# Kernel tuning notes

Hardware: AMD Instinct MI355X
Metric: run time of the kernel (lower is better)

The kernel has to match this reference:

```python
import jax, jax.numpy as jnp
import numpy as np

N_NODES = 15000
N_EDGES = 60000
NODE_VOCAB = 118 + 20000
EDGE_VOCAB = 4 + 50
NODE_INDIM = 64
EDGE_INDIM = 32
H = 32          # node_hidden_feats
EH = 64         # edge_hidden_feats
NUM_STEPS = 3   # num_step_message_passing
N_BOND_TYPES = 4  # edge ids < 4 are chemical bonds -> edge_func1, else knowledge relations -> edge_func2


def setup_inputs() -> dict:
    key = jax.random.key(0)
    ks = jax.random.split(key, 20)
    s = 0.05  # param scale for numerical stability
    return {
        "node_ids": jax.random.randint(ks[0], (N_NODES,), 0, NODE_VOCAB),
        "edge_ids": jax.random.randint(ks[1], (N_EDGES,), 0, EDGE_VOCAB),
        "src": jax.random.randint(ks[2], (N_EDGES,), 0, N_NODES),
        "dst": jax.random.randint(ks[3], (N_EDGES,), 0, N_NODES),
        "node_table": jax.random.normal(ks[4], (NODE_VOCAB, NODE_INDIM), jnp.float32),
        "edge_table": jax.random.normal(ks[5], (EDGE_VOCAB, EDGE_INDIM), jnp.float32),
        "proj_W": jax.random.normal(ks[6], (H, NODE_INDIM), jnp.float32) * s,
        "proj_b": jnp.zeros((H,), jnp.float32),
        "attn_w": jax.random.normal(ks[7], (2 * H,), jnp.float32) * s,
        "e1_W1": jax.random.normal(ks[8], (EH, EDGE_INDIM), jnp.float32) * s,
        "e1_b1": jnp.zeros((EH,), jnp.float32),
        "e1_W2": jax.random.normal(ks[9], (H * H, EH), jnp.float32) * s,
        "e1_b2": jnp.zeros((H * H,), jnp.float32),
        "e2_W1": jax.random.normal(ks[10], (EH, EDGE_INDIM), jnp.float32) * s,
        "e2_b1": jnp.zeros((EH,), jnp.float32),
        "e2_W2": jax.random.normal(ks[11], (H * H, EH), jnp.float32) * s,
        "e2_b2": jnp.zeros((H * H,), jnp.float32),
        "gru_Wih": jax.random.normal(ks[12], (3 * H, H), jnp.float32) * s,
        "gru_Whh": jax.random.normal(ks[13], (3 * H, H), jnp.float32) * s,
        "gru_bih": jnp.zeros((3 * H,), jnp.float32),
        "gru_bhh": jnp.zeros((3 * H,), jnp.float32),
    }


def _edge_softmax(logits, dst, num_nodes):
    # softmax over incoming edges of each destination node
    m = jax.ops.segment_max(logits, dst, num_segments=num_nodes)
    ex = jnp.exp(logits - m[dst])
    s = jax.ops.segment_sum(ex, dst, num_segments=num_nodes)
    return ex / s[dst]


def reference(node_ids, edge_ids, src, dst, node_table, edge_table, proj_W, proj_b,
              attn_w, e1_W1, e1_b1, e1_W2, e1_b2, e2_W1, e2_b1, e2_W2, e2_b2,
              gru_Wih, gru_Whh, gru_bih, gru_bhh):
    # --- embedding lookups ---
    nf = node_table[node_ids]                      # [N, node_indim]
    ef = edge_table[edge_ids]                      # [E, edge_indim]
    # --- project node feats: Linear + ReLU ---
    h = jax.nn.relu(nf @ proj_W.T + proj_b)        # [N, H]

    # --- per-edge weight matrices from the two edge MLPs (edge feats are
    # constant across message-passing steps, so compute once) ---
    def edge_mlp(W1, b1, W2, b2):
        z = jax.nn.relu(ef @ W1.T + b1)            # [E, EH]
        return (z @ W2.T + b2).reshape(-1, H, H)   # [E, H, H]

    W_e1 = edge_mlp(e1_W1, e1_b1, e1_W2, e1_b2)
    W_e2 = edge_mlp(e2_W1, e2_b1, e2_W2, e2_b2)
    is_bond = (edge_ids < N_BOND_TYPES)[:, None, None]
    W_edge = jnp.where(is_bond, W_e1, W_e2)        # [E, H, H]

    hidden = h                                     # GRU hidden state (seq of len 1 -> GRUCell)
    for _ in range(NUM_STEPS):
        # attention logits on edges: leaky_relu(attn_fc([h_src || h_dst]))
        a = jax.nn.leaky_relu(
            h[src] @ attn_w[:H] + h[dst] @ attn_w[H:])     # [E]
        alpha = _edge_softmax(a, dst, N_NODES)             # [E]
        # edge-conditioned message: (h_src @ W_e) weighted by attention
        msg = jnp.einsum('ei,eio->eo', h[src], W_edge) * alpha[:, None]  # [E, H]
        agg = jax.ops.segment_sum(msg, dst, num_segments=N_NODES)       # [N, H]
        m = jax.nn.relu(agg)
        # single GRU step (torch nn.GRU, 1 layer, seq_len 1)
        gi = m @ gru_Wih.T + gru_bih               # [N, 3H]
        gh = hidden @ gru_Whh.T + gru_bhh          # [N, 3H]
        ir, iz, inn = jnp.split(gi, 3, axis=1)
        hr, hz, hn = jnp.split(gh, 3, axis=1)
        r = jax.nn.sigmoid(ir + hr)
        z = jax.nn.sigmoid(iz + hz)
        n = jnp.tanh(inn + r * hn)
        hidden = (1.0 - z) * n + z * hidden
        h = hidden
    return h
```

## Files before the change

kernel.cpp:

```cpp
#include <hip/hip_runtime.h>
#include <math.h>

#define N_NODES   15000
#define N_EDGES   60000
#define EVOCAB    54
#define NODE_INDIM 64
#define EDGE_INDIM 32
#define H  32
#define EH 64
#define N_BOND 4

#define NPB   8
#define NBLK  (N_NODES / NPB)
#define CAP   128

#define TASK_VOCAB (EVOCAB * 1024)
#define TASK_PROJ  (N_NODES * H)
#define TASK_EDGE_BASE (TASK_VOCAB + TASK_PROJ)
#define TA_TOTAL   (TASK_EDGE_BASE + N_EDGES)

#define WT_OFF   0
#define H0_OFF   221184
#define H1_OFF   2141184
#define W4_OFF   4061184
#define W2_OFF   4077568
#define LS0_OFF  4085760
#define BS0_OFF  4145760
#define LS1_OFF  4205760
#define BS1_OFF  4265760
#define CNT_OFF  4325760
#define EPK_OFF  4333440
#define W2T1_OFF 5293440
#define W2T2_OFF 5555584
#define PT_OFF   5817728

__global__ __launch_bounds__(256)
void pre_kernel(const float* __restrict__ e1_W2, const float* __restrict__ e2_W2,
                const float* __restrict__ proj_W,
                const float* __restrict__ gWih, const float* __restrict__ gWhh,
                float* __restrict__ W2T1, float* __restrict__ W2T2,
                float* __restrict__ PT,
                float4* __restrict__ Wpk4, float2* __restrict__ Wpk2,
                int* __restrict__ cnt)
{
    int b = blockIdx.x, tid = threadIdx.x;
    if (b < 32) {
        __shared__ float st[64][65];
        const float* in = (b < 16) ? e1_W2 : e2_W2;
        float* out      = (b < 16) ? W2T1  : W2T2;
        int f0 = (b & 15) * 64;
        #pragma unroll
        for (int it = 0; it < 16; ++it) {
            int idx = it * 256 + tid;
            int r = idx >> 6, c = idx & 63;
            st[r][c] = in[(f0 + r) * 64 + c];
        }
        __syncthreads();
        #pragma unroll
        for (int it = 0; it < 16; ++it) {
            int idx = it * 256 + tid;
            int k = idx >> 6, f = idx & 63;
            out[k * 1024 + f0 + f] = st[f][k];
        }
    } else if (b == 32) {
        __shared__ float sp2[64][33];
        #pragma unroll
        for (int it = 0; it < 8; ++it) {
            int idx = it * 256 + tid;
            int o = idx >> 6, j = idx & 63;
            sp2[j][o] = proj_W[idx];
        }
        __syncthreads();
        #pragma unroll
        for (int it = 0; it < 8; ++it) {
            int idx = it * 256 + tid;
            int j = idx >> 5, o = idx & 31;
            PT[idx] = sp2[j][o];
        }
    } else if (b <= 36) {
        int q = (b - 33) * 256 + tid;
        int j = q >> 5, o = q & 31;
        Wpk4[q] = make_float4(gWih[o * 32 + j], gWih[(32 + o) * 32 + j],
                              gWih[(64 + o) * 32 + j], gWhh[o * 32 + j]);
        Wpk2[q] = make_float2(gWhh[(32 + o) * 32 + j], gWhh[(64 + o) * 32 + j]);
    } else {
        #pragma unroll
        for (int it = 0; it < 8; ++it) {
            int idx = it * 256 + tid;
            if (idx < NBLK) cnt[idx] = 0;
        }
    }
}

__global__ __launch_bounds__(256)
void setup_kernel(const int* __restrict__ node_ids, const int* __restrict__ src,
                  const int* __restrict__ dst, const int* __restrict__ eid,
                  const float* __restrict__ node_table, const float* __restrict__ edge_table,
                  const float* __restrict__ PT, const float* __restrict__ proj_b,
                  const float* __restrict__ attn_w,
                  const float* __restrict__ e1_W1, const float* __restrict__ e1_b1,
                  const float* __restrict__ e1_b2,
                  const float* __restrict__ e2_W1, const float* __restrict__ e2_b1,
                  const float* __restrict__ e2_b2,
                  const float* __restrict__ W2T1, const float* __restrict__ W2T2,
                  float* __restrict__ Wt, float* __restrict__ h0,
                  float* __restrict__ ls, float* __restrict__ bs,
                  int* __restrict__ cnt, int* __restrict__ blkE)
{
    int t = blockIdx.x * 256 + threadIdx.x;
    if (t >= TA_TOTAL) return;
    if (t < TASK_VOCAB) {
        int v = t >> 10, f = t & 1023, l = t & 63;
        const float* W1  = (v < N_BOND) ? e1_W1 : e2_W1;
        const float* b1  = (v < N_BOND) ? e1_b1 : e2_b1;
        const float* b2  = (v < N_BOND) ? e1_b2 : e2_b2;
        const float* W2T = (v < N_BOND) ? W2T1  : W2T2;
        const float4* ef4 = (const float4*)(edge_table + v * EDGE_INDIM);
        const float4* w14 = (const float4*)(W1 + l * EDGE_INDIM);
        float z = b1[l];
        #pragma unroll
        for (int j = 0; j < 8; ++j) {
            float4 a = ef4[j], b = w14[j];
            z += a.x*b.x + a.y*b.y + a.z*b.z + a.w*b.w;
        }
        z = fmaxf(z, 0.f);
        float y = b2[f];
        #pragma unroll 16
        for (int k = 0; k < 64; ++k)
            y += __shfl(z, k, 64) * W2T[k * 1024 + f];
        Wt[(v << 10) + f] = y;
    } else if (t < TASK_EDGE_BASE) {
        int q = t - TASK_VOCAB;
        int n = q >> 5, o = q & 31;
        int gid = node_ids[n];
        const float* nf = node_table + (size_t)gid * NODE_INDIM;
        float nfa = nf[o], nfb = nf[32 + o];
        float acc = proj_b[o];
        #pragma unroll 8
        for (int j = 0; j < 32; ++j)
            acc += __shfl(nfa, j, 32) * PT[j * 32 + o];
        #pragma unroll 8
        for (int j = 0; j < 32; ++j)
            acc += __shfl(nfb, j, 32) * PT[(32 + j) * 32 + o];
        float hval = fmaxf(acc, 0.f);
        h0[q] = hval;
        float c1 = hval * attn_w[o], c2 = hval * attn_w[32 + o];
        #pragma unroll
        for (int k = 16; k > 0; k >>= 1) {
            c1 += __shfl_xor(c1, k, 32);
            c2 += __shfl_xor(c2, k, 32);
        }
        if (o == 0) { ls[n] = c1; bs[n] = c2; }
    } else {
        int e = t - TASK_EDGE_BASE;
        int d = dst[e];
        int blk = d >> 3;
        int pack = src[e] | (eid[e] << 14) | ((d & 7) << 20);
        int slot = atomicAdd(&cnt[blk], 1);
        if (slot < CAP) blkE[blk * CAP + slot] = pack;
    }
}

__global__ __launch_bounds__(256)
void mp_kernel(const int* __restrict__ cnt, const int* __restrict__ blkE,
               const float* __restrict__ hc, const float* __restrict__ Wt,
               const float* __restrict__ attn_w,
               const float4* __restrict__ Wpk4, const float2* __restrict__ Wpk2,
               const float* __restrict__ gbih, const float* __restrict__ gbhh,
               const float* __restrict__ lsc, const float* __restrict__ bsc,
               float* __restrict__ lsn, float* __restrict__ bsn,
               float* __restrict__ op, int last)
{
    __shared__ float4 smsg4[CAP * 8];
    __shared__ float  sexs[CAP];
    __shared__ int    spk[CAP];
    __shared__ float  sbs[NPB];

    int b = blockIdx.x, tid = threadIdx.x;
    int cntB = cnt[b];
    if (cntB > CAP) cntB = CAP;
    if (tid < cntB) spk[tid] = blkE[b * CAP + tid];
    if (tid < NPB)  sbs[tid] = bsc[(b << 3) + tid];
    __syncthreads();

    int g = tid >> 5, o = tid & 31;

    for (int eb = 0; eb < cntB; eb += 16) {
        int e0 = eb + g, e1 = eb + 8 + g;
        float ex0 = 0.f; float4 p0 = make_float4(0.f, 0.f, 0.f, 0.f);
        if (e0 < cntB) {
            int pk = spk[e0];
            int sp = pk & 0x3FFF, vid = (pk >> 14) & 0x3F, dl = pk >> 20;
            float a = lsc[sp] + sbs[dl];
            a = (a > 0.f) ? a : 0.01f * a;
            ex0 = __expf(a);
            float hs = hc[(sp << 5) + o];
            const float4* W4 = (const float4*)(Wt + (vid << 10));
            #pragma unroll
            for (int k = 0; k < 8; ++k) {
                float4 w = W4[k * 32 + o];
                float hsk = __shfl(hs, 4 * k + (o >> 3), 32);
                p0.x += hsk * w.x; p0.y += hsk * w.y;
                p0.z += hsk * w.z; p0.w += hsk * w.w;
            }
        }
        float ex1 = 0.f; float4 p1 = make_float4(0.f, 0.f, 0.f, 0.f);
        if (e1 < cntB) {
            int pk = spk[e1];
            int sp = pk & 0x3FFF, vid = (pk >> 14) & 0x3F, dl = pk >> 20;
            float a = lsc[sp] + sbs[dl];
            a = (a > 0.f) ? a : 0.01f * a;
            ex1 = __expf(a);
            float hs = hc[(sp << 5) + o];
            const float4* W4 = (const float4*)(Wt + (vid << 10));
            #pragma unroll
            for (int k = 0; k < 8; ++k) {
                float4 w = W4[k * 32 + o];
                float hsk = __shfl(hs, 4 * k + (o >> 3), 32);
                p1.x += hsk * w.x; p1.y += hsk * w.y;
                p1.z += hsk * w.z; p1.w += hsk * w.w;
            }
        }
        p0.x += __shfl_xor(p0.x, 8, 32);  p0.y += __shfl_xor(p0.y, 8, 32);
        p0.z += __shfl_xor(p0.z, 8, 32);  p0.w += __shfl_xor(p0.w, 8, 32);
        p0.x += __shfl_xor(p0.x, 16, 32); p0.y += __shfl_xor(p0.y, 16, 32);
        p0.z += __shfl_xor(p0.z, 16, 32); p0.w += __shfl_xor(p0.w, 16, 32);
        p1.x += __shfl_xor(p1.x, 8, 32);  p1.y += __shfl_xor(p1.y, 8, 32);
        p1.z += __shfl_xor(p1.z, 8, 32);  p1.w += __shfl_xor(p1.w, 8, 32);
        p1.x += __shfl_xor(p1.x, 16, 32); p1.y += __shfl_xor(p1.y, 16, 32);
        p1.z += __shfl_xor(p1.z, 16, 32); p1.w += __shfl_xor(p1.w, 16, 32);
        if (e0 < cntB && o < 8) {
            smsg4[e0 * 8 + o] = make_float4(ex0 * p0.x, ex0 * p0.y, ex0 * p0.z, ex0 * p0.w);
            if (o == 0) sexs[e0] = ex0;
        }
        if (e1 < cntB && o < 8) {
            smsg4[e1 * 8 + o] = make_float4(ex1 * p1.x, ex1 * p1.y, ex1 * p1.z, ex1 * p1.w);
            if (o == 0) sexs[e1] = ex1;
        }
    }
    __syncthreads();

    const float* smsg = (const float*)smsg4;
    float sex = 0.f, acc = 0.f;
    for (int e = 0; e < cntB; ++e) {
        if ((spk[e] >> 20) == g) {
            acc += smsg[e * 32 + o];
            sex += sexs[e];
        }
    }
    float hv = hc[b * 256 + tid];
    float m = (sex != 0.f) ? fmaxf(acc / sex, 0.f) : 0.f;

    float gir = 0.f, giz = 0.f, gin = 0.f, ghr = 0.f, ghz = 0.f, ghn = 0.f;
    #pragma unroll 4
    for (int j = 0; j < 32; ++j) {
        float mj = __shfl(m, j, 32);
        float hj = __shfl(hv, j, 32);
        float4 a4 = Wpk4[j * 32 + o];
        float2 b2 = Wpk2[j * 32 + o];
        gir += mj * a4.x;  giz += mj * a4.y;  gin += mj * a4.z;
        ghr += hj * a4.w;  ghz += hj * b2.x;  ghn += hj * b2.y;
    }
    float r  = 1.f / (1.f + __expf(-(gir + gbih[o]      + ghr + gbhh[o])));
    float z  = 1.f / (1.f + __expf(-(giz + gbih[32 + o] + ghz + gbhh[32 + o])));
    float nn = tanhf(gin + gbih[64 + o] + r * (ghn + gbhh[64 + o]));
    float hid = (1.f - z) * nn + z * hv;
    op[b * 256 + tid] = hid;

    if (!last) {
        float c1 = hid * attn_w[o], c2 = hid * attn_w[32 + o];
        #pragma unroll
        for (int k = 16; k > 0; k >>= 1) {
            c1 += __shfl_xor(c1, k, 32);
            c2 += __shfl_xor(c2, k, 32);
        }
        if (o == 0) { lsn[(b << 3) + g] = c1; bsn[(b << 3) + g] = c2; }
    }
}

extern "C" void kernel_launch(void* const* d_in, const int* in_sizes, int n_in,
                              void* d_out, int out_size, void* d_ws, size_t ws_size,
                              hipStream_t stream) {
    const int*   node_ids   = (const int*)d_in[0];
    const int*   edge_ids   = (const int*)d_in[1];
    const int*   srcp       = (const int*)d_in[2];
    const int*   dstp       = (const int*)d_in[3];
    const float* node_table = (const float*)d_in[4];
    const float* edge_table = (const float*)d_in[5];
    const float* proj_W     = (const float*)d_in[6];
    const float* proj_b     = (const float*)d_in[7];
    const float* attn_w     = (const float*)d_in[8];
    const float* e1_W1 = (const float*)d_in[9];  const float* e1_b1 = (const float*)d_in[10];
    const float* e1_W2 = (const float*)d_in[11]; const float* e1_b2 = (const float*)d_in[12];
    const float* e2_W1 = (const float*)d_in[13]; const float* e2_b1 = (const float*)d_in[14];
    const float* e2_W2 = (const float*)d_in[15]; const float* e2_b2 = (const float*)d_in[16];
    const float* gWih  = (const float*)d_in[17]; const float* gWhh  = (const float*)d_in[18];
    const float* gbih  = (const float*)d_in[19]; const float* gbhh  = (const float*)d_in[20];
    float* outp = (float*)d_out;

    char* ws = (char*)d_ws;
    float*  Wt   = (float*)(ws + WT_OFF);
    float*  h0b  = (float*)(ws + H0_OFF);
    float*  h1b  = (float*)(ws + H1_OFF);
    float4* Wpk4 = (float4*)(ws + W4_OFF);
    float2* Wpk2 = (float2*)(ws + W2_OFF);
    float*  ls0  = (float*)(ws + LS0_OFF);
    float*  bs0  = (float*)(ws + BS0_OFF);
    float*  ls1  = (float*)(ws + LS1_OFF);
    float*  bs1  = (float*)(ws + BS1_OFF);
    int*    cnt  = (int*)  (ws + CNT_OFF);
    int*    blkE = (int*)  (ws + EPK_OFF);
    float*  W2T1 = (float*)(ws + W2T1_OFF);
    float*  W2T2 = (float*)(ws + W2T2_OFF);
    float*  PT   = (float*)(ws + PT_OFF);

    pre_kernel<<<38, 256, 0, stream>>>(
        e1_W2, e2_W2, proj_W, gWih, gWhh, W2T1, W2T2, PT, Wpk4, Wpk2, cnt);

    setup_kernel<<<(TA_TOTAL + 255) / 256, 256, 0, stream>>>(
        node_ids, srcp, dstp, edge_ids, node_table, edge_table, PT, proj_b,
        attn_w, e1_W1, e1_b1, e1_b2, e2_W1, e2_b1, e2_b2, W2T1, W2T2,
        Wt, h0b, ls0, bs0, cnt, blkE);

    float* hc = h0b;  float* hn = h1b;
    float* lc = ls0;  float* bc = bs0;
    float* ln = ls1;  float* bn = bs1;
    for (int step = 0; step < 3; ++step) {
        int last = (step == 2);
        float* op = last ? outp : hn;
        mp_kernel<<<NBLK, 256, 0, stream>>>(
            cnt, blkE, hc, Wt, attn_w, Wpk4, Wpk2, gbih, gbhh,
            lc, bc, ln, bn, op, last);
        float* tf;
        tf = hc; hc = hn; hn = tf;
        tf = lc; lc = ln; ln = tf;
        tf = bc; bc = bn; bn = tf;
    }
}
```

Baseline: 209.8 us.

## Bucket edges per destination node and process each node's edges in one wavefront half

Replaces the per-block edge bucket (8 nodes, cap 128) with per-node buckets of capacity 48, so each 32-lane group walks only its own node's incoming edges in registers. This removes the shared-memory message staging, the block barriers and the scan that matched every edge in the block against every node. Messages are now computed with a 32-step shuffle matvec, two edges at a time. The count buffer and workspace offsets grow to per-node size, and nodes with more than 48 in-edges would be silently truncated. Work now varies per lane group with each node's degree.

```diff
diff --git a/kernel.cpp b/kernel.cpp
--- a/kernel.cpp
+++ b/kernel.cpp
@@ -12,7 +12,7 @@
 
 #define NPB   8
 #define NBLK  (N_NODES / NPB)
-#define CAP   128
+#define CAPN  48
 
 #define TASK_VOCAB (EVOCAB * 1024)
 #define TASK_PROJ  (N_NODES * H)
@@ -29,10 +29,10 @@
 #define LS1_OFF  4205760
 #define BS1_OFF  4265760
 #define CNT_OFF  4325760
-#define EPK_OFF  4333440
-#define W2T1_OFF 5293440
-#define W2T2_OFF 5555584
-#define PT_OFF   5817728
+#define EPK_OFF  4385760
+#define W2T1_OFF 7265760
+#define W2T2_OFF 7527904
+#define PT_OFF   7790048
 
 __global__ __launch_bounds__(256)
 void pre_kernel(const float* __restrict__ e1_W2, const float* __restrict__ e2_W2,
@@ -84,11 +84,8 @@
                               gWih[(64 + o) * 32 + j], gWhh[o * 32 + j]);
         Wpk2[q] = make_float2(gWhh[(32 + o) * 32 + j], gWhh[(64 + o) * 32 + j]);
     } else {
-        #pragma unroll
-        for (int it = 0; it < 8; ++it) {
-            int idx = it * 256 + tid;
-            if (idx < NBLK) cnt[idx] = 0;
-        }
+        int idx = (b - 37) * 256 + tid;
+        if (idx < N_NODES) cnt[idx] = 0;
     }
 }
 
@@ -154,10 +151,9 @@
     } else {
         int e = t - TASK_EDGE_BASE;
         int d = dst[e];
-        int blk = d >> 3;
-        int pack = src[e] | (eid[e] << 14) | ((d & 7) << 20);
-        int slot = atomicAdd(&cnt[blk], 1);
-        if (slot < CAP) blkE[blk * CAP + slot] = pack;
+        int pack = src[e] | (eid[e] << 14);
+        int slot = atomicAdd(&cnt[d], 1);
+        if (slot < CAPN) blkE[d * CAPN + slot] = pack;
     }
 }
 
@@ -171,85 +167,54 @@
                float* __restrict__ lsn, float* __restrict__ bsn,
                float* __restrict__ op, int last)
 {
-    __shared__ float4 smsg4[CAP * 8];
-    __shared__ float  sexs[CAP];
-    __shared__ int    spk[CAP];
-    __shared__ float  sbs[NPB];
-
     int b = blockIdx.x, tid = threadIdx.x;
-    int cntB = cnt[b];
-    if (cntB > CAP) cntB = CAP;
-    if (tid < cntB) spk[tid] = blkE[b * CAP + tid];
-    if (tid < NPB)  sbs[tid] = bsc[(b << 3) + tid];
-    __syncthreads();
-
     int g = tid >> 5, o = tid & 31;
-
-    for (int eb = 0; eb < cntB; eb += 16) {
-        int e0 = eb + g, e1 = eb + 8 + g;
-        float ex0 = 0.f; float4 p0 = make_float4(0.f, 0.f, 0.f, 0.f);
-        if (e0 < cntB) {
-            int pk = spk[e0];
-            int sp = pk & 0x3FFF, vid = (pk >> 14) & 0x3F, dl = pk >> 20;
-            float a = lsc[sp] + sbs[dl];
-            a = (a > 0.f) ? a : 0.01f * a;
-            ex0 = __expf(a);
-            float hs = hc[(sp << 5) + o];
-            const float4* W4 = (const float4*)(Wt + (vid << 10));
-            #pragma unroll
-            for (int k = 0; k < 8; ++k) {
-                float4 w = W4[k * 32 + o];
-                float hsk = __shfl(hs, 4 * k + (o >> 3), 32);
-                p0.x += hsk * w.x; p0.y += hsk * w.y;
-                p0.z += hsk * w.z; p0.w += hsk * w.w;
-            }
-        }
-        float ex1 = 0.f; float4 p1 = make_float4(0.f, 0.f, 0.f, 0.f);
-        if (e1 < cntB) {
-            int pk = spk[e1];
-            int sp = pk & 0x3FFF, vid = (pk >> 14) & 0x3F, dl = pk >> 20;
-            float a = lsc[sp] + sbs[dl];
-            a = (a > 0.f) ? a : 0.01f * a;
-            ex1 = __expf(a);
-            float hs = hc[(sp << 5) + o];
-            const float4* W4 = (const float4*)(Wt + (vid << 10));
-            #pragma unroll
-            for (int k = 0; k < 8; ++k) {
-                float4 w = W4[k * 32 + o];
-                float hsk = __shfl(hs, 4 * k + (o >> 3), 32);
-                p1.x += hsk * w.x; p1.y += hsk * w.y;
-                p1.z += hsk * w.z; p1.w += hsk * w.w;
-            }
-        }
-        p0.x += __shfl_xor(p0.x, 8, 32);  p0.y += __shfl_xor(p0.y, 8, 32);
-        p0.z += __shfl_xor(p0.z, 8, 32);  p0.w += __shfl_xor(p0.w, 8, 32);
-        p0.x += __shfl_xor(p0.x, 16, 32); p0.y += __shfl_xor(p0.y, 16, 32);
-        p0.z += __shfl_xor(p0.z, 16, 32); p0.w += __shfl_xor(p0.w, 16, 32);
-        p1.x += __shfl_xor(p1.x, 8, 32);  p1.y += __shfl_xor(p1.y, 8, 32);
-        p1.z += __shfl_xor(p1.z, 8, 32);  p1.w += __shfl_xor(p1.w, 8, 32);
-        p1.x += __shfl_xor(p1.x, 16, 32); p1.y += __shfl_xor(p1.y, 16, 32);
-        p1.z += __shfl_xor(p1.z, 16, 32); p1.w += __shfl_xor(p1.w, 16, 32);
-        if (e0 < cntB && o < 8) {
-            smsg4[e0 * 8 + o] = make_float4(ex0 * p0.x, ex0 * p0.y, ex0 * p0.z, ex0 * p0.w);
-            if (o == 0) sexs[e0] = ex0;
-        }
-        if (e1 < cntB && o < 8) {
-            smsg4[e1 * 8 + o] = make_float4(ex1 * p1.x, ex1 * p1.y, ex1 * p1.z, ex1 * p1.w);
-            if (o == 0) sexs[e1] = ex1;
-        }
-    }
-    __syncthreads();
-
-    const float* smsg = (const float*)smsg4;
+    int n = (b << 3) + g;
+
+    int deg = cnt[n];
+    if (deg > CAPN) deg = CAPN;
+    int pks = blkE[n * CAPN + o];
+    float hv  = hc[(n << 5) + o];
+    float bdn = bsc[n];
+
     float sex = 0.f, acc = 0.f;
-    for (int e = 0; e < cntB; ++e) {
-        if ((spk[e] >> 20) == g) {
-            acc += smsg[e * 32 + o];
-            sex += sexs[e];
-        }
-    }
-    float hv = hc[b * 256 + tid];
-    float m = (sex != 0.f) ? fmaxf(acc / sex, 0.f) : 0.f;
+    int s = 0;
+    for (; s + 1 < deg; s += 2) {
+        int pk0 = __shfl(pks, s, 32);
+        int pk1 = __shfl(pks, s + 1, 32);
+        int sp0 = pk0 & 0x3FFF, v0 = pk0 >> 14;
+        int sp1 = pk1 & 0x3FFF, v1 = pk1 >> 14;
+        float a0 = lsc[sp0] + bdn; a0 = (a0 > 0.f) ? a0 : 0.01f * a0;
+        float a1 = lsc[sp1] + bdn; a1 = (a1 > 0.f) ? a1 : 0.01f * a1;
+        float ex0 = __expf(a0), ex1 = __expf(a1);
+        float hs0 = hc[(sp0 << 5) + o];
+        float hs1 = hc[(sp1 << 5) + o];
+        const float* W0 = Wt + (v0 << 10) + o;
+        const float* W1c = Wt + (v1 << 10) + o;
+        float y0 = 0.f, y1 = 0.f;
+        #pragma unroll
+        for (int i = 0; i < 32; ++i) {
+            y0 += __shfl(hs0, i, 32) * W0[i * 32];
+            y1 += __shfl(hs1, i, 32) * W1c[i * 32];
+        }
+        acc += ex0 * y0 + ex1 * y1;
+        sex += ex0 + ex1;
+    }
+    if (s < deg) {
+        int pk0 = __shfl(pks, s, 32);
+        int sp0 = pk0 & 0x3FFF, v0 = pk0 >> 14;
+        float a0 = lsc[sp0] + bdn; a0 = (a0 > 0.f) ? a0 : 0.01f * a0;
+        float ex0 = __expf(a0);
+        float hs0 = hc[(sp0 << 5) + o];
+        const float* W0 = Wt + (v0 << 10) + o;
+        float y0 = 0.f;
+        #pragma unroll
+        for (int i = 0; i < 32; ++i)
+            y0 += __shfl(hs0, i, 32) * W0[i * 32];
+        acc += ex0 * y0;
+        sex += ex0;
+    }
+    float m = (deg > 0) ? fmaxf(acc / sex, 0.f) : 0.f;
 
     float gir = 0.f, giz = 0.f, gin = 0.f, ghr = 0.f, ghz = 0.f, ghn = 0.f;
     #pragma unroll 4
@@ -265,7 +230,7 @@
     float z  = 1.f / (1.f + __expf(-(giz + gbih[32 + o] + ghz + gbhh[32 + o])));
     float nn = tanhf(gin + gbih[64 + o] + r * (ghn + gbhh[64 + o]));
     float hid = (1.f - z) * nn + z * hv;
-    op[b * 256 + tid] = hid;
+    op[(n << 5) + o] = hid;
 
     if (!last) {
         float c1 = hid * attn_w[o], c2 = hid * attn_w[32 + o];
@@ -274,7 +239,7 @@
             c1 += __shfl_xor(c1, k, 32);
             c2 += __shfl_xor(c2, k, 32);
         }
-        if (o == 0) { lsn[(b << 3) + g] = c1; bsn[(b << 3) + g] = c2; }
+        if (o == 0) { lsn[n] = c1; bsn[n] = c2; }
     }
 }
 
@@ -314,7 +279,7 @@
     float*  W2T2 = (float*)(ws + W2T2_OFF);
     float*  PT   = (float*)(ws + PT_OFF);
 
-    pre_kernel<<<38, 256, 0, stream>>>(
+    pre_kernel<<<96, 256, 0, stream>>>(
         e1_W2, e2_W2, proj_W, gWih, gWhh, W2T1, W2T2, PT, Wpk4, Wpk2, cnt);
 
     setup_kernel<<<(TA_TOTAL + 255) / 256, 256, 0, stream>>>(
```

Result: slower. 219.2 us (+4.5%).
